# Optimization experiments

Hardware: AMD Instinct MI355X
Metric: run time of the kernel (lower is better)

## Reference

```python
import jax, jax.numpy as jnp
import numpy as np
import math

H = 32       # num_attention_heads
HKV = 8      # num_key_value_heads
D = 128      # attention_head_size


def setup_inputs() -> dict:
    key = jax.random.key(0)
    k1, k2, k3 = jax.random.split(key, 3)
    B, L = 2, 2048
    return {
        "query_states": jax.random.normal(k1, (B, L, H * D), dtype=jnp.float32),
        "key_states": jax.random.normal(k2, (B, L, HKV * D), dtype=jnp.float32),
        "value_states": jax.random.normal(k3, (B, L, HKV * D), dtype=jnp.float32),
    }


def reference(query_states, key_states, value_states):
    B, L, _ = query_states.shape
    groups = H // HKV

    # view + transpose(1,2): (B, heads, L, D)
    q = query_states.reshape(B, L, H, D).transpose(0, 2, 1, 3)
    k = key_states.reshape(B, L, HKV, D).transpose(0, 2, 1, 3)
    v = value_states.reshape(B, L, HKV, D).transpose(0, 2, 1, 3)

    # repeat_kv: repeat_interleave along head dim
    k = jnp.repeat(k, groups, axis=1)
    v = jnp.repeat(v, groups, axis=1)

    q = q.astype(jnp.float16)
    k = k.astype(jnp.float16)
    v = v.astype(jnp.float16)

    # source: transpose(1,2) -> (B, L, H, D), then reshape(B*H, L, D)
    # (row-major reshape of the (B,L,H,D) layout, replicated exactly)
    q = q.transpose(0, 2, 1, 3).reshape(B * H, L, D)
    k = k.transpose(0, 2, 1, 3).reshape(B * H, L, D)
    v = v.transpose(0, 2, 1, 3).reshape(B * H, L, D)

    scale = 1.0 / math.sqrt(D)
    attn_scores = jnp.einsum("bqd,bkd->bqk", q, k) * jnp.float16(scale)
    attn_weights = jax.nn.softmax(attn_scores, axis=-1)
    attn_output = jnp.einsum("bqk,bkd->bqd", attn_weights, v)

    # reshape(B,H,L,D).transpose(1,2) -> (B,L,H,D) -> (B, L, H*D)
    attn_output = attn_output.reshape(B, H, L, D).transpose(0, 2, 1, 3)
    return attn_output.reshape(B, L, H * D)
```

## Files before the change

kernel.cpp:

```cpp
#include <hip/hip_runtime.h>

typedef _Float16 f16;
typedef f16 f16x2 __attribute__((ext_vector_type(2)));
typedef f16 f16x4 __attribute__((ext_vector_type(4)));
typedef f16 f16x8 __attribute__((ext_vector_type(8)));
typedef float f32x4 __attribute__((ext_vector_type(4)));

#define NB   2
#define LL   2048
#define LQ   2048
#define LKV  512
#define DD   128
#define BM   128
#define BN   64
#define NKT  (LKV/BN)
#define PT_STR 68
#define KS_STR 132
#define VT_STR 68

#define G_STRIDE 65536ull
#define WS_BYTES (2ull*64ull*G_STRIDE*2ull)

#define GLOAD16(gsrc, ldst) \
    __builtin_amdgcn_global_load_lds((const __attribute__((address_space(1))) void*)(gsrc), \
                                     (__attribute__((address_space(3))) void*)(ldst), 16, 0, 0)

__global__ __launch_bounds__(256)
void prepack(const float* __restrict__ kg, const float* __restrict__ vg,
             f16* __restrict__ ws)
{
    __shared__ float vtile[64*132];
    const int tid = threadIdx.x;
    const int kt  = blockIdx.x;
    const int g   = blockIdx.y;

    if (blockIdx.z == 0) {
        const float* kb = kg + (size_t)g*65536 + (size_t)kt*8192;
        f16* kout = ws + (size_t)g*G_STRIDE + (size_t)kt*8192;
#pragma unroll
        for (int i = 0; i < 4; ++i) {
            int q = i*256 + tid;
            int r = q >> 4, c = q & 15;
            const float* src = kb + r*128 + ((c ^ (r&7))*8);
            float4 a = *(const float4*)src;
            float4 b = *(const float4*)(src + 4);
            f16x8 h = { (f16)a.x,(f16)a.y,(f16)a.z,(f16)a.w,
                        (f16)b.x,(f16)b.y,(f16)b.z,(f16)b.w };
            *(f16x8*)(kout + (size_t)q*8) = h;
        }
    } else {
        const float* vb = vg + (size_t)g*65536 + (size_t)kt*8192;
        f16* vout = ws + 64ull*G_STRIDE + (size_t)g*G_STRIDE + (size_t)kt*8192;
#pragma unroll
        for (int i = 0; i < 8; ++i) {
            int f = tid + i*256;
            int row = f >> 5, c4 = f & 31;
            float4 x = *(const float4*)(vb + (size_t)f*4);
            *(float4*)(vtile + row*132 + c4*4) = x;
        }
        __syncthreads();
#pragma unroll
        for (int i = 0; i < 4; ++i) {
            int q = i*256 + tid;
            int r = q >> 3, c = q & 7;
            int kv0 = (c ^ (r&7))*8;
            f16x8 h;
#pragma unroll
            for (int j = 0; j < 8; ++j) h[j] = (f16)vtile[(kv0+j)*132 + r];
            *(f16x8*)(vout + (size_t)q*8) = h;
        }
    }
}

__global__ __launch_bounds__(256, 3)
void fa_fwd(const float* __restrict__ qg, const f16* __restrict__ ws,
            float* __restrict__ og)
{
    __shared__ __align__(16) f16 Ks[BN*DD];
    __shared__ __align__(16) f16 Vt[DD*BN];
    __shared__ __align__(16) f16 Pt[BM*PT_STR];

    const int tid  = threadIdx.x;
    const int wave = tid >> 6;
    const int lane = tid & 63;
    const int ln   = lane & 15;
    const int qd   = lane >> 4;

    const int bid = blockIdx.x;
    const int qt  = (bid >> 3) & 15;
    const int g   = ((bid & 7) << 3) | (bid >> 7);
    const int bb  = g >> 5;
    const int lhi = g & 31;

    const float* qmat = qg + (size_t)(bb*LL + 64*lhi)*4096;
    const f16*   kw   = ws + (size_t)g*G_STRIDE;
    const f16*   vw   = ws + (64ull + (size_t)g)*G_STRIDE;

    const int qbase = qt*BM + wave*32;

    auto issueK = [&](int kt) {
#pragma unroll
        for (int i = 0; i < 4; ++i)
            GLOAD16(kw + (size_t)kt*8192 + (size_t)(i*256 + tid)*8,
                    Ks + (i*256 + wave*64)*8);
    };
    auto issueV = [&](int kt) {
#pragma unroll
        for (int i = 0; i < 4; ++i)
            GLOAD16(vw + (size_t)kt*8192 + (size_t)(i*256 + tid)*8,
                    Vt + (i*256 + wave*64)*8);
    };

    issueK(0);
    issueV(0);

    f16x8 qf[2][4];
#pragma unroll
    for (int nt = 0; nt < 2; ++nt) {
        const float* qrow = qmat + (size_t)(qbase + 16*nt + ln)*DD;
#pragma unroll
        for (int kc = 0; kc < 4; ++kc) {
            const float4* qp = (const float4*)(qrow + kc*32 + 8*qd);
            float4 f0 = qp[0], f1 = qp[1];
            f16x8 t = { (f16)f0.x,(f16)f0.y,(f16)f0.z,(f16)f0.w,
                        (f16)f1.x,(f16)f1.y,(f16)f1.z,(f16)f1.w };
            qf[nt][kc] = t;
        }
    }

    f32x4 o[2][8];
#pragma unroll
    for (int nt = 0; nt < 2; ++nt)
#pragma unroll
        for (int dmt = 0; dmt < 8; ++dmt)
#pragma unroll
            for (int r = 0; r < 4; ++r) o[nt][dmt][r] = 0.0f;

    float mrun[2] = {-1e30f, -1e30f}, lrun[2] = {0.0f, 0.0f};
    const float SC2 = 0.08837890625f * 1.44269504088896340f;

    __syncthreads();

#pragma unroll 1
    for (int t = 0; t < NKT; ++t) {
        f32x4 st[2][4];
#pragma unroll
        for (int nt = 0; nt < 2; ++nt)
#pragma unroll
            for (int mt = 0; mt < 4; ++mt)
#pragma unroll
                for (int r = 0; r < 4; ++r) st[nt][mt][r] = 0.0f;
#pragma unroll
        for (int mt = 0; mt < 4; ++mt) {
            const int R = 16*mt + ln;
#pragma unroll
            for (int kc = 0; kc < 4; ++kc) {
                f16x8 af = *(const f16x8*)(Ks + R*DD + (((kc*4 + qd) ^ (R&7))*8));
#pragma unroll
                for (int nt = 0; nt < 2; ++nt)
                    st[nt][mt] = __builtin_amdgcn_mfma_f32_16x16x32_f16(af, qf[nt][kc], st[nt][mt], 0,0,0);
            }
        }

        float alph[2];
#pragma unroll
        for (int nt = 0; nt < 2; ++nt) {
            float mx = -1e30f;
#pragma unroll
            for (int mt = 0; mt < 4; ++mt)
#pragma unroll
                for (int r = 0; r < 4; ++r) {
                    float v = st[nt][mt][r]*SC2; st[nt][mt][r] = v; mx = fmaxf(mx, v);
                }
            mx = fmaxf(mx, __shfl_xor(mx, 16, 64));
            mx = fmaxf(mx, __shfl_xor(mx, 32, 64));
            float mnew = fmaxf(mrun[nt], mx);
            alph[nt] = exp2f(mrun[nt] - mnew);
            float rs = 0.0f;
#pragma unroll
            for (int mt = 0; mt < 4; ++mt)
#pragma unroll
                for (int r = 0; r < 4; ++r) {
                    float p = exp2f(st[nt][mt][r] - mnew);
                    st[nt][mt][r] = p; rs += p;
                }
            rs += __shfl_xor(rs, 16, 64);
            rs += __shfl_xor(rs, 32, 64);
            lrun[nt] = lrun[nt]*alph[nt] + rs;
            mrun[nt] = mnew;
        }

#pragma unroll
        for (int nt = 0; nt < 2; ++nt) {
            f16* prow = Pt + (wave*32 + 16*nt + ln)*PT_STR + 4*qd;
#pragma unroll
            for (int mt = 0; mt < 4; ++mt)
#pragma unroll
                for (int p2 = 0; p2 < 2; ++p2) {
                    f16x2 pp = { (f16)st[nt][mt][2*p2], (f16)st[nt][mt][2*p2+1] };
                    *(f16x2*)(prow + 16*mt + 2*p2) = pp;
                }
        }

        __syncthreads();
        if (t+1 < NKT) issueK(t+1);

#pragma unroll
        for (int nt = 0; nt < 2; ++nt)
#pragma unroll
            for (int dmt = 0; dmt < 8; ++dmt)
#pragma unroll
                for (int r = 0; r < 4; ++r) o[nt][dmt][r] *= alph[nt];

#pragma unroll
        for (int kc2 = 0; kc2 < 2; ++kc2) {
            f16x8 pf[2];
#pragma unroll
            for (int nt = 0; nt < 2; ++nt) {
                const f16* pr = Pt + (wave*32 + 16*nt + ln)*PT_STR + kc2*32 + 8*qd;
                f16x4 b0 = *(const f16x4*)(pr);
                f16x4 b1 = *(const f16x4*)(pr + 4);
                pf[nt] = __builtin_shufflevector(b0, b1, 0,1,2,3,4,5,6,7);
            }
#pragma unroll
            for (int dmt = 0; dmt < 8; ++dmt) {
                const int R = 16*dmt + ln;
                f16x8 vf = *(const f16x8*)(Vt + R*BN + (((kc2*4 + qd) ^ (R&7))*8));
#pragma unroll
                for (int nt = 0; nt < 2; ++nt)
                    o[nt][dmt] = __builtin_amdgcn_mfma_f32_16x16x32_f16(vf, pf[nt], o[nt][dmt], 0,0,0);
            }
        }

        __syncthreads();
        if (t+1 < NKT) issueV(t+1);
    }

#pragma unroll
    for (int nt = 0; nt < 2; ++nt) {
        float inv = 1.0f / lrun[nt];
        int qtok = qbase + 16*nt + ln;
        float* orow = og + (size_t)(bb*LL + qtok)*4096 + lhi*DD + 4*qd;
#pragma unroll
        for (int dmt = 0; dmt < 8; ++dmt) {
            float4 x = { o[nt][dmt][0]*inv, o[nt][dmt][1]*inv,
                         o[nt][dmt][2]*inv, o[nt][dmt][3]*inv };
            *(float4*)(orow + 16*dmt) = x;
        }
    }
}

__global__ __launch_bounds__(256, 2)
void fa_fwd_fb(const float* __restrict__ qg,
               const float* __restrict__ kg,
               const float* __restrict__ vg,
               float* __restrict__ og)
{
    __shared__ __align__(16) f16 smem[BN*KS_STR + DD*VT_STR + BM*PT_STR];
    f16* Ks = smem;
    f16* Vt = smem + BN*KS_STR;
    f16* Pt = smem + BN*KS_STR + DD*VT_STR;

    const int tid  = threadIdx.x;
    const int wave = tid >> 6;
    const int lane = tid & 63;
    const int ln   = lane & 15;
    const int qd   = lane >> 4;

    const int qt   = blockIdx.x;
    const int g    = blockIdx.y;
    const int bb   = g >> 5;
    const int lhi  = g & 31;

    const float* qmat = qg + (size_t)(bb*LL + 64*lhi)*4096;
    const float* kmat = kg + (size_t)(bb*LL + 64*lhi)*1024;
    const float* vmat = vg + (size_t)(bb*LL + 64*lhi)*1024;

    const int qbase = qt*BM + wave*32;

    f16x8 qf[2][4];
#pragma unroll
    for (int nt = 0; nt < 2; ++nt) {
        const float* qrow = qmat + (size_t)(qbase + 16*nt + ln)*DD;
#pragma unroll
        for (int kc = 0; kc < 4; ++kc) {
            const float4* qp = (const float4*)(qrow + kc*32 + 8*qd);
            float4 f0 = qp[0], f1 = qp[1];
            f16x8 t = { (f16)f0.x,(f16)f0.y,(f16)f0.z,(f16)f0.w,
                        (f16)f1.x,(f16)f1.y,(f16)f1.z,(f16)f1.w };
            qf[nt][kc] = t;
        }
    }

    f32x4 o[2][8];
#pragma unroll
    for (int nt = 0; nt < 2; ++nt)
#pragma unroll
        for (int dmt = 0; dmt < 8; ++dmt)
#pragma unroll
            for (int r = 0; r < 4; ++r) o[nt][dmt][r] = 0.0f;

    float mrun[2] = {-1e30f, -1e30f}, lrun[2] = {0.0f, 0.0f};
    const float SC2 = 0.08837890625f * 1.44269504088896340f;

    for (int kt = 0; kt < LKV/BN; ++kt) {
        const float* kb = kmat + kt*BN*DD;
        const float* vb = vmat + kt*BN*DD;

#pragma unroll
        for (int i = 0; i < 8; ++i) {
            int f = tid + i*256;
            int row = f >> 5, c4 = f & 31;
            float4 x = *(const float4*)(kb + f*4);
            f16x4 h4 = { (f16)x.x,(f16)x.y,(f16)x.z,(f16)x.w };
            *(f16x4*)(Ks + row*KS_STR + c4*4) = h4;
        }
#pragma unroll
        for (int i = 0; i < 8; ++i) {
            int f = tid + i*256;
            int kvr = f & 63, c4 = f >> 6;
            float4 x = *(const float4*)(vb + (size_t)kvr*DD + c4*4);
            Vt[(c4*4+0)*VT_STR + kvr] = (f16)x.x;
            Vt[(c4*4+1)*VT_STR + kvr] = (f16)x.y;
            Vt[(c4*4+2)*VT_STR + kvr] = (f16)x.z;
            Vt[(c4*4+3)*VT_STR + kvr] = (f16)x.w;
        }
        __syncthreads();

        f32x4 st[2][4];
#pragma unroll
        for (int nt = 0; nt < 2; ++nt)
#pragma unroll
            for (int mt = 0; mt < 4; ++mt)
#pragma unroll
                for (int r = 0; r < 4; ++r) st[nt][mt][r] = 0.0f;
#pragma unroll
        for (int mt = 0; mt < 4; ++mt) {
            const f16* kr = Ks + (16*mt + ln)*KS_STR + 8*qd;
#pragma unroll
            for (int kc = 0; kc < 4; ++kc) {
                f16x4 a0 = *(const f16x4*)(kr + kc*32);
                f16x4 a1 = *(const f16x4*)(kr + kc*32 + 4);
                f16x8 af = __builtin_shufflevector(a0, a1, 0,1,2,3,4,5,6,7);
#pragma unroll
                for (int nt = 0; nt < 2; ++nt)
                    st[nt][mt] = __builtin_amdgcn_mfma_f32_16x16x32_f16(af, qf[nt][kc], st[nt][mt], 0,0,0);
            }
        }

        float alph[2];
#pragma unroll
        for (int nt = 0; nt < 2; ++nt) {
            float mx = -1e30f;
#pragma unroll
            for (int mt = 0; mt < 4; ++mt)
#pragma unroll
                for (int r = 0; r < 4; ++r) {
                    float v = st[nt][mt][r]*SC2; st[nt][mt][r] = v; mx = fmaxf(mx, v);
                }
            mx = fmaxf(mx, __shfl_xor(mx, 16, 64));
            mx = fmaxf(mx, __shfl_xor(mx, 32, 64));
            float mnew = fmaxf(mrun[nt], mx);
            alph[nt] = exp2f(mrun[nt] - mnew);
            float rs = 0.0f;
#pragma unroll
            for (int mt = 0; mt < 4; ++mt)
#pragma unroll
                for (int r = 0; r < 4; ++r) {
                    float p = exp2f(st[nt][mt][r] - mnew);
                    st[nt][mt][r] = p; rs += p;
                }
            rs += __shfl_xor(rs, 16, 64);
            rs += __shfl_xor(rs, 32, 64);
            lrun[nt] = lrun[nt]*alph[nt] + rs;
            mrun[nt] = mnew;
        }

#pragma unroll
        for (int nt = 0; nt < 2; ++nt) {
            f16* prow = Pt + (wave*32 + 16*nt + ln)*PT_STR + 4*qd;
#pragma unroll
            for (int mt = 0; mt < 4; ++mt)
#pragma unroll
                for (int p2 = 0; p2 < 2; ++p2) {
                    f16x2 pp = { (f16)st[nt][mt][2*p2], (f16)st[nt][mt][2*p2+1] };
                    *(f16x2*)(prow + 16*mt + 2*p2) = pp;
                }
        }

#pragma unroll
        for (int nt = 0; nt < 2; ++nt)
#pragma unroll
            for (int dmt = 0; dmt < 8; ++dmt)
#pragma unroll
                for (int r = 0; r < 4; ++r) o[nt][dmt][r] *= alph[nt];

#pragma unroll
        for (int kc2 = 0; kc2 < 2; ++kc2) {
            f16x8 pf[2];
#pragma unroll
            for (int nt = 0; nt < 2; ++nt) {
                const f16* pr = Pt + (wave*32 + 16*nt + ln)*PT_STR + kc2*32 + 8*qd;
                f16x4 b0 = *(const f16x4*)(pr);
                f16x4 b1 = *(const f16x4*)(pr + 4);
                pf[nt] = __builtin_shufflevector(b0, b1, 0,1,2,3,4,5,6,7);
            }
#pragma unroll
            for (int dmt = 0; dmt < 8; ++dmt) {
                const f16* vr = Vt + (16*dmt + ln)*VT_STR + kc2*32 + 8*qd;
                f16x4 a0 = *(const f16x4*)(vr);
                f16x4 a1 = *(const f16x4*)(vr + 4);
                f16x8 vf = __builtin_shufflevector(a0, a1, 0,1,2,3,4,5,6,7);
#pragma unroll
                for (int nt = 0; nt < 2; ++nt)
                    o[nt][dmt] = __builtin_amdgcn_mfma_f32_16x16x32_f16(vf, pf[nt], o[nt][dmt], 0,0,0);
            }
        }
        __syncthreads();
    }

#pragma unroll
    for (int nt = 0; nt < 2; ++nt) {
        float inv = 1.0f / lrun[nt];
        int qtok = qbase + 16*nt + ln;
        float* orow = og + (size_t)(bb*LL + qtok)*4096 + lhi*DD + 4*qd;
#pragma unroll
        for (int dmt = 0; dmt < 8; ++dmt) {
            float4 x = { o[nt][dmt][0]*inv, o[nt][dmt][1]*inv,
                         o[nt][dmt][2]*inv, o[nt][dmt][3]*inv };
            *(float4*)(orow + 16*dmt) = x;
        }
    }
}

extern "C" void kernel_launch(void* const* d_in, const int* in_sizes, int n_in,
                              void* d_out, int out_size, void* d_ws, size_t ws_size,
                              hipStream_t stream) {
    (void)in_sizes; (void)n_in; (void)out_size;
    const float* q = (const float*)d_in[0];
    const float* k = (const float*)d_in[1];
    const float* v = (const float*)d_in[2];
    float* o = (float*)d_out;
    if (d_ws != nullptr && ws_size >= (size_t)WS_BYTES) {
        hipLaunchKernelGGL(prepack, dim3(8, 64, 2), dim3(256), 0, stream,
                           k, v, (f16*)d_ws);
        hipLaunchKernelGGL(fa_fwd, dim3(1024), dim3(256), 0, stream,
                           q, (const f16*)d_ws, o);
    } else {
        hipLaunchKernelGGL(fa_fwd_fb, dim3(LQ/BM, 64), dim3(256), 0, stream,
                           q, k, v, o);
    }
}
```

Measured before the change: 218.0 us.

## Read K and V fragments directly from global memory instead of staging in LDS

The prepack kernel now writes K in plain row-major f16 and V transposed as a contiguous [D][LKV] matrix, dropping the XOR swizzle. The attention kernel removes the LDS staging buffers for K and V, the async global-to-LDS loads and the block barriers, and loads MFMA operands straight from global memory through the cache. It also raises wave priority around the MFMA loops. This removes barrier and LDS traffic but exposes global and L2 latency on every fragment load, with no prefetch to hide it.

```diff
diff --git a/kernel.cpp b/kernel.cpp
--- a/kernel.cpp
+++ b/kernel.cpp
@@ -21,10 +21,6 @@
 #define G_STRIDE 65536ull
 #define WS_BYTES (2ull*64ull*G_STRIDE*2ull)
 
-#define GLOAD16(gsrc, ldst) \
-    __builtin_amdgcn_global_load_lds((const __attribute__((address_space(1))) void*)(gsrc), \
-                                     (__attribute__((address_space(3))) void*)(ldst), 16, 0, 0)
-
 __global__ __launch_bounds__(256)
 void prepack(const float* __restrict__ kg, const float* __restrict__ vg,
              f16* __restrict__ ws)
@@ -38,19 +34,15 @@
         const float* kb = kg + (size_t)g*65536 + (size_t)kt*8192;
         f16* kout = ws + (size_t)g*G_STRIDE + (size_t)kt*8192;
 #pragma unroll
-        for (int i = 0; i < 4; ++i) {
-            int q = i*256 + tid;
-            int r = q >> 4, c = q & 15;
-            const float* src = kb + r*128 + ((c ^ (r&7))*8);
-            float4 a = *(const float4*)src;
-            float4 b = *(const float4*)(src + 4);
-            f16x8 h = { (f16)a.x,(f16)a.y,(f16)a.z,(f16)a.w,
-                        (f16)b.x,(f16)b.y,(f16)b.z,(f16)b.w };
-            *(f16x8*)(kout + (size_t)q*8) = h;
+        for (int i = 0; i < 8; ++i) {
+            int f = tid + i*256;
+            float4 x = *(const float4*)(kb + (size_t)f*4);
+            f16x4 h = { (f16)x.x,(f16)x.y,(f16)x.z,(f16)x.w };
+            *(f16x4*)(kout + (size_t)f*4) = h;
         }
     } else {
         const float* vb = vg + (size_t)g*65536 + (size_t)kt*8192;
-        f16* vout = ws + 64ull*G_STRIDE + (size_t)g*G_STRIDE + (size_t)kt*8192;
+        f16* vout = ws + 64ull*G_STRIDE + (size_t)g*G_STRIDE;
 #pragma unroll
         for (int i = 0; i < 8; ++i) {
             int f = tid + i*256;
@@ -63,11 +55,10 @@
         for (int i = 0; i < 4; ++i) {
             int q = i*256 + tid;
             int r = q >> 3, c = q & 7;
-            int kv0 = (c ^ (r&7))*8;
             f16x8 h;
 #pragma unroll
-            for (int j = 0; j < 8; ++j) h[j] = (f16)vtile[(kv0+j)*132 + r];
-            *(f16x8*)(vout + (size_t)q*8) = h;
+            for (int j = 0; j < 8; ++j) h[j] = (f16)vtile[(c*8+j)*132 + r];
+            *(f16x8*)(vout + (size_t)r*LKV + kt*64 + c*8) = h;
         }
     }
 }
@@ -76,8 +67,6 @@
 void fa_fwd(const float* __restrict__ qg, const f16* __restrict__ ws,
             float* __restrict__ og)
 {
-    __shared__ __align__(16) f16 Ks[BN*DD];
-    __shared__ __align__(16) f16 Vt[DD*BN];
     __shared__ __align__(16) f16 Pt[BM*PT_STR];
 
     const int tid  = threadIdx.x;
@@ -97,22 +86,6 @@
     const f16*   vw   = ws + (64ull + (size_t)g)*G_STRIDE;
 
     const int qbase = qt*BM + wave*32;
-
-    auto issueK = [&](int kt) {
-#pragma unroll
-        for (int i = 0; i < 4; ++i)
-            GLOAD16(kw + (size_t)kt*8192 + (size_t)(i*256 + tid)*8,
-                    Ks + (i*256 + wave*64)*8);
-    };
-    auto issueV = [&](int kt) {
-#pragma unroll
-        for (int i = 0; i < 4; ++i)
-            GLOAD16(vw + (size_t)kt*8192 + (size_t)(i*256 + tid)*8,
-                    Vt + (i*256 + wave*64)*8);
-    };
-
-    issueK(0);
-    issueV(0);
 
     f16x8 qf[2][4];
 #pragma unroll
@@ -139,8 +112,6 @@
     float mrun[2] = {-1e30f, -1e30f}, lrun[2] = {0.0f, 0.0f};
     const float SC2 = 0.08837890625f * 1.44269504088896340f;
 
-    __syncthreads();
-
 #pragma unroll 1
     for (int t = 0; t < NKT; ++t) {
         f32x4 st[2][4];
@@ -150,17 +121,19 @@
             for (int mt = 0; mt < 4; ++mt)
 #pragma unroll
                 for (int r = 0; r < 4; ++r) st[nt][mt][r] = 0.0f;
+        __builtin_amdgcn_s_setprio(1);
 #pragma unroll
         for (int mt = 0; mt < 4; ++mt) {
-            const int R = 16*mt + ln;
+            const f16* kr = kw + (size_t)(t*BN + 16*mt + ln)*DD + 8*qd;
 #pragma unroll
             for (int kc = 0; kc < 4; ++kc) {
-                f16x8 af = *(const f16x8*)(Ks + R*DD + (((kc*4 + qd) ^ (R&7))*8));
+                f16x8 af = *(const f16x8*)(kr + kc*32);
 #pragma unroll
                 for (int nt = 0; nt < 2; ++nt)
                     st[nt][mt] = __builtin_amdgcn_mfma_f32_16x16x32_f16(af, qf[nt][kc], st[nt][mt], 0,0,0);
             }
         }
+        __builtin_amdgcn_s_setprio(0);
 
         float alph[2];
 #pragma unroll
@@ -202,9 +175,6 @@
                 }
         }
 
-        __syncthreads();
-        if (t+1 < NKT) issueK(t+1);
-
 #pragma unroll
         for (int nt = 0; nt < 2; ++nt)
 #pragma unroll
@@ -222,18 +192,17 @@
                 f16x4 b1 = *(const f16x4*)(pr + 4);
                 pf[nt] = __builtin_shufflevector(b0, b1, 0,1,2,3,4,5,6,7);
             }
+            __builtin_amdgcn_s_setprio(1);
 #pragma unroll
             for (int dmt = 0; dmt < 8; ++dmt) {
-                const int R = 16*dmt + ln;
-                f16x8 vf = *(const f16x8*)(Vt + R*BN + (((kc2*4 + qd) ^ (R&7))*8));
+                f16x8 vf = *(const f16x8*)(vw + (size_t)(16*dmt + ln)*LKV
+                                              + t*BN + kc2*32 + 8*qd);
 #pragma unroll
                 for (int nt = 0; nt < 2; ++nt)
                     o[nt][dmt] = __builtin_amdgcn_mfma_f32_16x16x32_f16(vf, pf[nt], o[nt][dmt], 0,0,0);
             }
-        }
-
-        __syncthreads();
-        if (t+1 < NKT) issueV(t+1);
+            __builtin_amdgcn_s_setprio(0);
+        }
     }
 
 #pragma unroll
```

After: 278.3 us. +27.6%, slower.

## Keep softmax probabilities in registers by permuting K rows to match MFMA layout

Applied to the files above, without the earlier changes.

Drops the shared-memory P tile. K rows are permuted in the QK^T MFMA so that each lane's score accumulator already matches the B-operand layout of the PV MFMA, which lets P be converted to f16 in registers with no LDS round trip. The K and V swizzle function changes to match the new row mapping, and s_setprio brackets the MFMA loops. This removes the LDS writes and reads for P and frees LDS, but correctness depends on the permutation and swizzle being consistent between prepack and consumer.

```diff
diff --git a/kernel.cpp b/kernel.cpp
--- a/kernel.cpp
+++ b/kernel.cpp
@@ -14,12 +14,14 @@
 #define BM   128
 #define BN   64
 #define NKT  (LKV/BN)
-#define PT_STR 68
 #define KS_STR 132
 #define VT_STR 68
+#define PT_STR 68
 
 #define G_STRIDE 65536ull
 #define WS_BYTES (2ull*64ull*G_STRIDE*2ull)
+
+__device__ inline int swz3(int r) { return (r & 3) | ((r & 8) >> 1); }
 
 #define GLOAD16(gsrc, ldst) \
     __builtin_amdgcn_global_load_lds((const __attribute__((address_space(1))) void*)(gsrc), \
@@ -41,7 +43,7 @@
         for (int i = 0; i < 4; ++i) {
             int q = i*256 + tid;
             int r = q >> 4, c = q & 15;
-            const float* src = kb + r*128 + ((c ^ (r&7))*8);
+            const float* src = kb + r*128 + ((c ^ swz3(r))*8);
             float4 a = *(const float4*)src;
             float4 b = *(const float4*)(src + 4);
             f16x8 h = { (f16)a.x,(f16)a.y,(f16)a.z,(f16)a.w,
@@ -63,7 +65,7 @@
         for (int i = 0; i < 4; ++i) {
             int q = i*256 + tid;
             int r = q >> 3, c = q & 7;
-            int kv0 = (c ^ (r&7))*8;
+            int kv0 = (c ^ swz3(r))*8;
             f16x8 h;
 #pragma unroll
             for (int j = 0; j < 8; ++j) h[j] = (f16)vtile[(kv0+j)*132 + r];
@@ -78,7 +80,6 @@
 {
     __shared__ __align__(16) f16 Ks[BN*DD];
     __shared__ __align__(16) f16 Vt[DD*BN];
-    __shared__ __align__(16) f16 Pt[BM*PT_STR];
 
     const int tid  = threadIdx.x;
     const int wave = tid >> 6;
@@ -150,17 +151,19 @@
             for (int mt = 0; mt < 4; ++mt)
 #pragma unroll
                 for (int r = 0; r < 4; ++r) st[nt][mt][r] = 0.0f;
+        __builtin_amdgcn_s_setprio(1);
 #pragma unroll
         for (int mt = 0; mt < 4; ++mt) {
-            const int R = 16*mt + ln;
+            const int R = 32*(mt >> 1) + 8*(ln >> 2) + 4*(mt & 1) + (ln & 3);
 #pragma unroll
             for (int kc = 0; kc < 4; ++kc) {
-                f16x8 af = *(const f16x8*)(Ks + R*DD + (((kc*4 + qd) ^ (R&7))*8));
+                f16x8 af = *(const f16x8*)(Ks + R*DD + (((kc*4 + qd) ^ swz3(R))*8));
 #pragma unroll
                 for (int nt = 0; nt < 2; ++nt)
                     st[nt][mt] = __builtin_amdgcn_mfma_f32_16x16x32_f16(af, qf[nt][kc], st[nt][mt], 0,0,0);
             }
         }
+        __builtin_amdgcn_s_setprio(0);
 
         float alph[2];
 #pragma unroll
@@ -190,18 +193,6 @@
             mrun[nt] = mnew;
         }
 
-#pragma unroll
-        for (int nt = 0; nt < 2; ++nt) {
-            f16* prow = Pt + (wave*32 + 16*nt + ln)*PT_STR + 4*qd;
-#pragma unroll
-            for (int mt = 0; mt < 4; ++mt)
-#pragma unroll
-                for (int p2 = 0; p2 < 2; ++p2) {
-                    f16x2 pp = { (f16)st[nt][mt][2*p2], (f16)st[nt][mt][2*p2+1] };
-                    *(f16x2*)(prow + 16*mt + 2*p2) = pp;
-                }
-        }
-
         __syncthreads();
         if (t+1 < NKT) issueK(t+1);
 
@@ -217,19 +208,22 @@
             f16x8 pf[2];
 #pragma unroll
             for (int nt = 0; nt < 2; ++nt) {
-                const f16* pr = Pt + (wave*32 + 16*nt + ln)*PT_STR + kc2*32 + 8*qd;
-                f16x4 b0 = *(const f16x4*)(pr);
-                f16x4 b1 = *(const f16x4*)(pr + 4);
-                pf[nt] = __builtin_shufflevector(b0, b1, 0,1,2,3,4,5,6,7);
-            }
+                f16x8 pp = { (f16)st[nt][2*kc2+0][0], (f16)st[nt][2*kc2+0][1],
+                             (f16)st[nt][2*kc2+0][2], (f16)st[nt][2*kc2+0][3],
+                             (f16)st[nt][2*kc2+1][0], (f16)st[nt][2*kc2+1][1],
+                             (f16)st[nt][2*kc2+1][2], (f16)st[nt][2*kc2+1][3] };
+                pf[nt] = pp;
+            }
+            __builtin_amdgcn_s_setprio(1);
 #pragma unroll
             for (int dmt = 0; dmt < 8; ++dmt) {
                 const int R = 16*dmt + ln;
-                f16x8 vf = *(const f16x8*)(Vt + R*BN + (((kc2*4 + qd) ^ (R&7))*8));
+                f16x8 vf = *(const f16x8*)(Vt + R*BN + (((kc2*4 + qd) ^ swz3(R))*8));
 #pragma unroll
                 for (int nt = 0; nt < 2; ++nt)
                     o[nt][dmt] = __builtin_amdgcn_mfma_f32_16x16x32_f16(vf, pf[nt], o[nt][dmt], 0,0,0);
             }
+            __builtin_amdgcn_s_setprio(0);
         }
 
         __syncthreads();
```

Result: faster. 202.4 us (-7.2%).
